# Kernel optimization log

Hardware: AMD Instinct MI355X
Metric: run time of the kernel (lower is better)

## Reference

```python
import jax, jax.numpy as jnp
import numpy as np

B, FEW, NSN, NQ, NN = 256, 5, 5, 10, 512
M, D, H, L, NSYM = 200, 100, 450, 2, 70000
BETA, MARGIN = 5.0, 1.0


def _lstm_dir(x, W_ih, W_hh, b_ih, b_hh):
    # x: (T, B, in) -> outputs (T, B, H), final h (B, H). PyTorch gate order i,f,g,o.
    Bn, Hn = x.shape[1], W_hh.shape[1]
    def cell(carry, xt):
        h, c = carry
        g = xt @ W_ih.T + h @ W_hh.T + b_ih + b_hh
        i, f, gg, o = jnp.split(g, 4, axis=-1)
        c = jax.nn.sigmoid(f) * c + jax.nn.sigmoid(i) * jnp.tanh(gg)
        h = jax.nn.sigmoid(o) * jnp.tanh(c)
        return (h, c), h
    z = jnp.zeros((Bn, Hn), x.dtype)
    (hT, _), ys = jax.lax.scan(cell, (z, z), x)
    return ys, hT


def _bidir(x, Wih, Whh, bih, bhh):
    # Wih: (2, 4H, in) stacked [fwd, bwd]
    yf, hf = _lstm_dir(x, Wih[0], Whh[0], bih[0], bhh[0])
    yb, hb = _lstm_dir(x[::-1], Wih[1], Whh[1], bih[1], bhh[1])
    return jnp.concatenate([yf, yb[::-1]], -1), hf, hb


def setup_inputs():
    key = jax.random.key(0)
    ks = jax.random.split(key, 30)
    f32 = jnp.float32
    emb = jax.random.normal(ks[0], (NSYM + 1, D), f32) * 0.1
    emb = emb.at[NSYM].set(0.0)  # padding_idx
    s = 0.05
    inp = dict(
        support=jax.random.normal(ks[1], (B, FEW, 2, D), f32),
        support_negative=jax.random.normal(ks[2], (B, NSN, 2, D), f32),
        query=jax.random.normal(ks[3], (B, NQ, 2, D), f32),
        negative=jax.random.normal(ks[4], (B, NN, 2, D), f32),
        norm_vector=jax.random.normal(ks[5], (B, 1, 1, D), f32),
        left_conn=jax.random.randint(ks[6], (FEW, B, M, 3), 0, NSYM, jnp.int32),
        right_conn=jax.random.randint(ks[7], (FEW, B, M, 3), 0, NSYM, jnp.int32),
        symbol_emb=emb,
        gcn_w=jax.random.normal(ks[8], (D, 2 * D), f32) * s,
        gcn_wb=jnp.zeros((D,), f32),
        gcn_b=jnp.zeros((D,), f32),
        attn_w=jax.random.normal(ks[9], (1, D), f32) * s,
        attn_wb=jnp.zeros((1,), f32),
        gate_w=jax.random.normal(ks[10], (1, D), f32) * s,
        gate_wb=jnp.zeros((1,), f32),
        gate_b=jnp.zeros((1,), f32),
        Wih0=jax.random.normal(ks[11], (2, 4 * H, 2 * D), f32) * s,
        Whh0=jax.random.normal(ks[12], (2, 4 * H, H), f32) * s,
        bih0=jnp.zeros((2, 4 * H), f32),
        bhh0=jnp.zeros((2, 4 * H), f32),
        Wih1=jax.random.normal(ks[13], (2, 4 * H, 2 * H), f32) * s,
        Whh1=jax.random.normal(ks[14], (2, 4 * H, H), f32) * s,
        bih1=jnp.zeros((2, 4 * H), f32),
        bhh1=jnp.zeros((2, 4 * H), f32),
        out_w=jax.random.normal(ks[15], (D, 2 * H * L), f32) * s,
        out_b=jnp.zeros((D,), f32),
    )
    return inp


def reference(support, support_negative, query, negative, norm_vector,
              left_conn, right_conn, symbol_emb,
              gcn_w, gcn_wb, gcn_b, attn_w, attn_wb, gate_w, gate_wb, gate_b,
              Wih0, Whh0, bih0, bhh0, Wih1, Whh1, bih1, bhh1, out_w, out_b):
    few, b, m, _ = left_conn.shape
    d = symbol_emb.shape[1]

    def neighbor_encoder(conn):  # (N, M, 3) -> (N, D); dropout=identity (eval)
        rel_e = symbol_emb[conn[:, :, 1]]            # (N, M, D)
        ent_e = symbol_emb[conn[:, :, 2]]            # (N, M, D)
        self_e = symbol_emb[conn[:, 0, 0]]           # (N, D)
        cat = jnp.concatenate([rel_e, ent_e], -1)    # (N, M, 2D)
        out = jax.nn.leaky_relu(cat @ gcn_w.T + gcn_wb + gcn_b, 0.01)
        attn = jax.nn.softmax(out @ attn_w.T + attn_wb, axis=1)  # (N, M, 1)
        out_attn = jnp.einsum('nmd,nm->nd', out, attn[..., 0])
        gate = jax.nn.sigmoid(out_attn @ gate_w.T + gate_wb + gate_b)  # (N, 1)
        return out_attn * gate + self_e * (1.0 - gate)

    # all (few, left/right) encodings in one fused pass
    conn_all = jnp.stack([left_conn, right_conn], 1).reshape(few * 2 * b, m, 3)
    enc = neighbor_encoder(conn_all).reshape(few, 2, b, d).transpose(2, 0, 1, 3)  # (B, few, 2, D)

    # LSTM_attn relation learner
    x = enc.reshape(b, few, 2 * d).transpose(1, 0, 2)  # (T=few, B, 2D)
    y, h0f, h0b = _bidir(x, Wih0, Whh0, bih0, bhh0)
    y, h1f, h1b = _bidir(y, Wih1, Whh1, bih1, bhh1)
    final = jnp.stack([h0f, h0b, h1f, h1b], 0)         # (2*L, B, H)
    output = y.transpose(1, 0, 2)                       # (B, T, 2H)
    hidden = final.reshape(-1, 2 * H, L)                # faithful to torch .view
    aw = jax.nn.softmax(jnp.einsum('bth,bhl->btl', output, hidden), axis=1)
    context = jnp.einsum('bth,btl->bhl', output, aw).reshape(b, 2 * H * L)
    rel = (context @ out_w.T + out_b).reshape(b, 1, 1, d)

    def split_concat(pos, neg):
        e1 = jnp.concatenate([pos[:, :, 0, :], neg[:, :, 0, :]], 1)[:, :, None, :]
        e2 = jnp.concatenate([pos[:, :, 1, :], neg[:, :, 1, :]], 1)[:, :, None, :]
        return e1, e2

    def emb_learner(h, t, r, norm, pos_num):
        norm = norm[:, :1, :, :]
        h = h - jnp.sum(h * norm, -1, keepdims=True) * norm
        t = t - jnp.sum(t * norm, -1, keepdims=True) * norm
        score = -jnp.linalg.norm(h + r - t, axis=-1)[:, :, 0]
        return score[:, :pos_num], score[:, pos_num:]

    nsn = support_negative.shape[1]
    def inner_loss(rel_):
        rel_s = jnp.broadcast_to(rel_, (b, few + nsn, 1, d))
        e1, e2 = split_concat(support, support_negative)
        p, n = emb_learner(e1, e2, rel_s, norm_vector, few)
        return jnp.mean(jax.nn.relu(MARGIN - (p - n)))

    grad_meta = jax.grad(inner_loss)(rel)
    rel_q = rel - BETA * grad_meta
    norm_q = norm_vector - BETA * grad_meta

    nq, nn = query.shape[1], negative.shape[1]
    e1, e2 = split_concat(query, negative)
    rel_qe = jnp.broadcast_to(rel_q, (b, nq + nn, 1, d))
    p_score, n_score = emb_learner(e1, e2, rel_qe, norm_q, nq)
    return p_score, n_score
```

## Files before the change

kernel.cpp:

```cpp
#include <hip/hip_runtime.h>

typedef unsigned short u16;
typedef unsigned int   u32;
typedef __attribute__((ext_vector_type(8))) short short8;
typedef __attribute__((ext_vector_type(4))) float f32x4;

__device__ __forceinline__ float u2f(u32 u){
  union { u32 i; float f; } v; v.i = u << 16; return v.f;
}
__device__ __forceinline__ u16 f2bu(float f){
  union { float f; u32 i; } v; v.f = f;
  u32 i = v.i;
  i += 0x7fffu + ((i >> 16) & 1u);
  return (u16)(i >> 16);
}
__device__ __forceinline__ float sigm(float x){ return 1.0f/(1.0f + expf(-x)); }
__device__ __forceinline__ float ldf(const void* p, size_t i, int bf){
  return bf ? u2f(((const u16*)p)[i]) : ((const float*)p)[i];
}
__device__ __forceinline__ float wsum(float v){
  #pragma unroll
  for (int off = 32; off > 0; off >>= 1) v += __shfl_xor(v, off, 64);
  return v;
}

__global__ __launch_bounds__(64) void k_detect(const u32* __restrict__ nv,
                                               int* __restrict__ flag)
{
  int i = threadIdx.x;
  u32 w = nv[i];
  u32 e = (w >> 7) & 0xffu;
  bool sane = (e >= 100u && e <= 140u);
  unsigned long long m = __ballot(sane);
  if (i == 0) *flag = (__popcll(m) >= 40) ? 1 : 0;
}

__global__ __launch_bounds__(256) void k_pack(
    const void* __restrict__ src, u16* __restrict__ dst,
    int K, int Kp, int R, int Rp, const int* __restrict__ flag)
{
  const int bf = *flag;
  int total = Rp*Kp;
  int idx = blockIdx.x*256 + threadIdx.x;
  if (idx >= total) return;
  int r = idx / Kp, k = idx - r*Kp;
  u16 v = 0;
  if (k < K && r < R){
    size_t si = (size_t)r*K + k;
    v = bf ? ((const u16*)src)[si] : f2bu(((const float*)src)[si]);
  }
  dst[idx] = v;
}

__global__ __launch_bounds__(256) void k_packe(
    const void* __restrict__ emb, u16* __restrict__ Eb,
    int total4, const int* __restrict__ flag)
{
  const int bf = *flag;
  int idx = blockIdx.x*256 + threadIdx.x;
  if (idx >= total4) return;
  size_t i = (size_t)idx*4;
  union { u16 q[4]; uint2 d; } o;
  if (bf){
    o.d = *(const uint2*)((const u16*)emb + i);
  } else {
    float4 t = *(const float4*)((const float*)emb + i);
    o.q[0] = f2bu(t.x); o.q[1] = f2bu(t.y);
    o.q[2] = f2bu(t.z); o.q[3] = f2bu(t.w);
  }
  *(uint2*)(Eb + i) = o.d;
}

__global__ __launch_bounds__(256) void k_packg(
    const void* __restrict__ src, u16* __restrict__ dst,
    int K, int Kp, const int* __restrict__ flag)
{
  const int bf = *flag;
  const int Kq = Kp >> 2;
  const int per = 1920*Kq;
  int idx = blockIdx.x*256 + threadIdx.x;
  if (idx >= 2*per) return;
  int z = idx / per, r = idx - z*per;
  int rp = r / Kq, cq = r - rp*Kq;
  int c0 = cq*4;
  int kblk = rp >> 6, rem = rp & 63, gate = rem >> 4, klo = rem & 15;
  int k = kblk*16 + klo;
  union { u16 q[4]; uint2 d; } o;
  o.q[0] = 0; o.q[1] = 0; o.q[2] = 0; o.q[3] = 0;
  if (k < 450){
    size_t base = ((size_t)z*1800 + (size_t)gate*450 + k)*K;
    #pragma unroll
    for (int e = 0; e < 4; ++e){
      int c = c0 + e;
      if (c < K)
        o.q[e] = bf ? ((const u16*)src)[base+c] : f2bu(((const float*)src)[base+c]);
    }
  }
  *(uint2*)(dst + (size_t)idx*4) = o.d;
}

__global__ __launch_bounds__(256) void k_packb(
    const void* __restrict__ bih, const void* __restrict__ bhh,
    float* __restrict__ Bp, const int* __restrict__ flag)
{
  const int bf = *flag;
  int idx = blockIdx.x*256 + threadIdx.x;
  if (idx >= 2*1920) return;
  int z = idx / 1920, rp = idx - z*1920;
  int kblk = rp >> 6, rem = rp & 63, gate = rem >> 4, klo = rem & 15;
  int k = kblk*16 + klo;
  float v = 0.0f;
  if (k < 450){
    size_t si = (size_t)z*1800 + (size_t)gate*450 + k;
    v = ldf(bih, si, bf) + ldf(bhh, si, bf);
  }
  Bp[idx] = v;
}

__global__ __launch_bounds__(512, 4) void k_gcn(
    const int* __restrict__ left, const int* __restrict__ right,
    const void* __restrict__ emb, const u16* __restrict__ Eb,
    const u16* __restrict__ Wg,
    const void* __restrict__ gcnwb, const void* __restrict__ gcnb,
    const void* __restrict__ attnw, const void* __restrict__ attnwb,
    const void* __restrict__ gatew, const void* __restrict__ gatewb,
    const void* __restrict__ gateb,
    const int* __restrict__ flag,
    u16* __restrict__ X0bf)
{
  __shared__ __align__(16) u16 As[208*40];
  __shared__ __align__(16) u16 Bs[112*232];
  __shared__ int c1_s[200], c2_s[200];
  __shared__ float logit_s[208];
  __shared__ float red_s[512];
  __shared__ float attnw_s[112], bias_s[112], gatew_s[112], oa_s[112];

  const int bf  = *flag;
  const int tid = threadIdx.x;
  const int n   = blockIdx.x;
  const int b   = n & 255;
  const int fs  = n >> 8;
  const int s   = fs & 1;
  const int f   = fs >> 1;
  const int* conn = (s == 0 ? left : right) + (size_t)(f*256 + b)*600;

  if (tid < 200){ c1_s[tid] = conn[tid*3+1]; c2_s[tid] = conn[tid*3+2]; }
  if (tid < 112){
    attnw_s[tid] = (tid < 100) ? ldf(attnw, tid, bf) : 0.0f;
    bias_s[tid]  = (tid < 100) ? (ldf(gcnwb, tid, bf) + ldf(gcnb, tid, bf)) : 0.0f;
    gatew_s[tid] = (tid < 100) ? ldf(gatew, tid, bf) : 0.0f;
    oa_s[tid] = 0.0f;
  }
  for (int g = tid; g < 112*28; g += 512){
    int r = g / 28, cc = g - r*28;
    *(short8*)(Bs + r*232 + cc*8) = *(const short8*)(Wg + (size_t)r*224 + cc*8);
  }
  __syncthreads();

  const int wid  = tid >> 6, lane = tid & 63, ln = lane & 15, quad = lane >> 4;
  const int mt0 = (wid < 5) ? 2*wid : (10 + (wid - 5));
  const int nmt = (wid < 5) ? 2 : 1;

  auto loadA = [&](int kc, uint2* pv){
    #pragma unroll
    for (int it = 0; it < 4; ++it){
      int g = tid + it*512;
      uint2 v; v.x = 0u; v.y = 0u;
      if (g < 1664){
        int r = g >> 3, gi = g & 7, k = kc*32 + gi*4;
        if (r < 200 && k < 200){
          int c  = (k < 100) ? c1_s[r] : c2_s[r];
          int kk = (k < 100) ? k : (k - 100);
          v = *(const uint2*)(Eb + (size_t)c*100 + kk);
        }
      }
      pv[it] = v;
    }
  };

  f32x4 acc[2][7];
  #pragma unroll
  for (int i = 0; i < 2; ++i)
    #pragma unroll
    for (int j = 0; j < 7; ++j) acc[i][j] = (f32x4)0.0f;

  uint2 pv[4];
  loadA(0, pv);

  for (int kc = 0; kc < 7; ++kc){
    const int k0 = kc*32;
    #pragma unroll
    for (int it = 0; it < 4; ++it){
      int g = tid + it*512;
      if (g < 1664){
        int r = g >> 3, gi = g & 7;
        *(uint2*)(As + r*40 + gi*4) = pv[it];
      }
    }
    __syncthreads();
    if (kc < 6) loadA(kc+1, pv);

    #pragma unroll
    for (int mi = 0; mi < 2; ++mi){
      if (mi < nmt){
        short8 afr = *(const short8*)(As + ((mt0+mi)*16 + ln)*40 + quad*8);
        #pragma unroll
        for (int nt = 0; nt < 7; ++nt){
          short8 bfr = *(const short8*)(Bs + (size_t)(nt*16 + ln)*232 + k0 + quad*8);
          acc[mi][nt] = __builtin_amdgcn_mfma_f32_16x16x32_bf16(afr, bfr, acc[mi][nt], 0, 0, 0);
        }
      }
    }
    __syncthreads();
  }

  const float awb = ldf(attnwb, 0, bf);
  #pragma unroll
  for (int mi = 0; mi < 2; ++mi){
    if (mi < nmt){
      #pragma unroll
      for (int rg = 0; rg < 4; ++rg){
        float p = 0.0f;
        #pragma unroll
        for (int nt = 0; nt < 7; ++nt){
          float x = acc[mi][nt][rg] + bias_s[nt*16 + ln];
          x = x > 0.0f ? x : 0.01f*x;
          p += x * attnw_s[nt*16 + ln];
        }
        p += __shfl_xor(p, 1, 64); p += __shfl_xor(p, 2, 64);
        p += __shfl_xor(p, 4, 64); p += __shfl_xor(p, 8, 64);
        int m = (mt0+mi)*16 + quad*4 + rg;
        if (ln == 0 && m < 200) logit_s[m] = p + awb;
      }
    }
  }
  __syncthreads();

  red_s[tid] = (tid < 200) ? logit_s[tid] : -3.0e38f;
  __syncthreads();
  for (int off = 256; off > 0; off >>= 1){
    if (tid < off) red_s[tid] = fmaxf(red_s[tid], red_s[tid+off]);
    __syncthreads();
  }
  float mx = red_s[0];
  __syncthreads();
  float ev = 0.0f;
  if (tid < 200) ev = expf(logit_s[tid] - mx);
  red_s[tid] = ev;
  __syncthreads();
  for (int off = 256; off > 0; off >>= 1){
    if (tid < off) red_s[tid] += red_s[tid+off];
    __syncthreads();
  }
  float S = red_s[0];
  __syncthreads();
  if (tid < 208) logit_s[tid] = (tid < 200) ? ev*(1.0f/S) : 0.0f;
  __syncthreads();

  float at[2][4];
  #pragma unroll
  for (int mi = 0; mi < 2; ++mi)
    #pragma unroll
    for (int rg = 0; rg < 4; ++rg)
      at[mi][rg] = (mi < nmt) ? logit_s[(mt0+mi)*16 + quad*4 + rg] : 0.0f;

  #pragma unroll
  for (int nt = 0; nt < 7; ++nt){
    float p = 0.0f;
    #pragma unroll
    for (int mi = 0; mi < 2; ++mi){
      if (mi < nmt){
        #pragma unroll
        for (int rg = 0; rg < 4; ++rg){
          float x = acc[mi][nt][rg] + bias_s[nt*16 + ln];
          x = x > 0.0f ? x : 0.01f*x;
          p += x * at[mi][rg];
        }
      }
    }
    p += __shfl_xor(p, 16, 64); p += __shfl_xor(p, 32, 64);
    if (quad == 0) atomicAdd(&oa_s[nt*16 + ln], p);
  }
  __syncthreads();

  red_s[tid] = (tid < 100) ? oa_s[tid]*gatew_s[tid] : 0.0f;
  __syncthreads();
  for (int off = 256; off > 0; off >>= 1){
    if (tid < off) red_s[tid] += red_s[tid+off];
    __syncthreads();
  }
  float gate = sigm(red_s[0] + ldf(gatewb, 0, bf) + ldf(gateb, 0, bf));
  if (tid < 100){
    int c0 = conn[0];
    float self = ldf(emb, (size_t)c0*100 + tid, bf);
    X0bf[((size_t)f*256 + b)*224 + s*100 + tid] = f2bu(oa_s[tid]*gate + self*(1.0f - gate));
  }
}

__global__ __launch_bounds__(256) void k_mgemm(
    const u16* __restrict__ A, int lda, size_t Astride,
    const u16* __restrict__ B, int ldb, size_t Bstride,
    const float* __restrict__ bsum,
    u16* __restrict__ out, size_t Ostride,
    int N, int KC)
{
  __shared__ __align__(16) u16 As[128*40];
  __shared__ __align__(16) u16 Bs[128*40];
  const int tid = threadIdx.x;
  const int z  = blockIdx.z;
  const int nb = blockIdx.x, mb = blockIdx.y;
  const u16* Az = A + (size_t)z*Astride;
  const u16* Bz = B + (size_t)z*Bstride;

  const int wid = tid >> 6, lane = tid & 63, ln = lane & 15, quad = lane >> 4;
  const int wm = wid >> 1, wn = wid & 1;

  f32x4 acc[4][4];
  #pragma unroll
  for (int i = 0; i < 4; ++i)
    #pragma unroll
    for (int j = 0; j < 4; ++j) acc[i][j] = (f32x4)0.0f;

  const int srow = tid >> 1;
  const int koff = (tid & 1)*16;
  const int rowA = mb*128 + srow;
  const int rowB = nb*128 + srow;

  for (int kc = 0; kc < KC; ++kc){
    const int k0 = kc*32 + koff;
    const u16* ap = Az + (size_t)rowA*lda + k0;
    const u16* bp = Bz + (size_t)rowB*ldb + k0;
    short8 av0 = *(const short8*)(ap);
    short8 av1 = *(const short8*)(ap + 8);
    short8 bv0 = *(const short8*)(bp);
    short8 bv1 = *(const short8*)(bp + 8);
    *(short8*)(As + srow*40 + koff)     = av0;
    *(short8*)(As + srow*40 + koff + 8) = av1;
    *(short8*)(Bs + srow*40 + koff)     = bv0;
    *(short8*)(Bs + srow*40 + koff + 8) = bv1;
    __syncthreads();
    short8 af[4], bfr[4];
    #pragma unroll
    for (int i = 0; i < 4; ++i)
      af[i] = *(const short8*)(As + (wm*64 + i*16 + ln)*40 + quad*8);
    #pragma unroll
    for (int j = 0; j < 4; ++j)
      bfr[j] = *(const short8*)(Bs + (wn*64 + j*16 + ln)*40 + quad*8);
    #pragma unroll
    for (int i = 0; i < 4; ++i)
      #pragma unroll
      for (int j = 0; j < 4; ++j)
        acc[i][j] = __builtin_amdgcn_mfma_f32_16x16x32_bf16(af[i], bfr[j], acc[i][j], 0, 0, 0);
    __syncthreads();
  }

  #pragma unroll
  for (int j = 0; j < 4; ++j){
    int col = nb*128 + wn*64 + j*16 + ln;
    float bias = bsum ? bsum[(size_t)z*1920 + col] : 0.0f;
    #pragma unroll
    for (int i = 0; i < 4; ++i){
      #pragma unroll
      for (int rg = 0; rg < 4; ++rg){
        int row = mb*128 + wm*64 + i*16 + quad*4 + rg;
        out[(size_t)z*Ostride + (size_t)row*N + col] = f2bu(acc[i][j][rg] + bias);
      }
    }
  }
}

__global__ __launch_bounds__(256) void k_hstep(
    const u16* __restrict__ Hin, const u16* __restrict__ Whp,
    const u16* __restrict__ Gb, float* __restrict__ HC,
    u16* __restrict__ Hout, u16* __restrict__ Ybf, float* __restrict__ Yf,
    float* __restrict__ HF, int s, int layer)
{
  __shared__ __align__(16) u16 As[32*40];
  __shared__ __align__(16) u16 Bs[128*40];
  const int tid = threadIdx.x;
  const int nb = blockIdx.x, mb = blockIdx.y, z = blockIdx.z;
  const int wid = tid >> 6, lane = tid & 63, ln = lane & 15, quad = lane >> 4;
  const int wm = wid >> 1, wn = wid & 1;

  const u16* Az = Hin + ((size_t)z*256 + mb*32)*480;
  const u16* Bz = Whp + (size_t)z*1920*480 + (size_t)nb*128*480;

  f32x4 acc[4];
  #pragma unroll
  for (int j = 0; j < 4; ++j) acc[j] = (f32x4)0.0f;

  const int ar = tid >> 2, ap = tid & 3;
  const int br = tid >> 1, bp = tid & 1;
  for (int kc = 0; kc < 15; ++kc){
    const int k0 = kc*32;
    if (tid < 128)
      *(short8*)(As + ar*40 + ap*8) = *(const short8*)(Az + (size_t)ar*480 + k0 + ap*8);
    *(short8*)(Bs + br*40 + bp*16)     = *(const short8*)(Bz + (size_t)br*480 + k0 + bp*16);
    *(short8*)(Bs + br*40 + bp*16 + 8) = *(const short8*)(Bz + (size_t)br*480 + k0 + bp*16 + 8);
    __syncthreads();
    short8 afr = *(const short8*)(As + (wm*16 + ln)*40 + quad*8);
    #pragma unroll
    for (int j = 0; j < 4; ++j){
      short8 bfr = *(const short8*)(Bs + (wn*64 + j*16 + ln)*40 + quad*8);
      acc[j] = __builtin_amdgcn_mfma_f32_16x16x32_bf16(afr, bfr, acc[j], 0, 0, 0);
    }
    __syncthreads();
  }

  const int kblk = nb*2 + wn;
  const int k = kblk*16 + ln;
  const int t = z ? (4 - s) : s;
  if (k < 450){
    const u16* Gz = Gb + (size_t)z*2457600 + (size_t)t*256*1920;
    #pragma unroll
    for (int rg = 0; rg < 4; ++rg){
      int b = mb*32 + wm*16 + quad*4 + rg;
      const u16* grow = Gz + (size_t)b*1920 + nb*128 + wn*64 + ln;
      float gi = acc[0][rg] + u2f(grow[0]);
      float gf = acc[1][rg] + u2f(grow[16]);
      float gg = acc[2][rg] + u2f(grow[32]);
      float go = acc[3][rg] + u2f(grow[48]);
      float* cp = HC + ((size_t)(2+z)*256 + b)*450 + k;
      float c = sigm(gf)*(*cp) + sigm(gi)*tanhf(gg);
      float h = sigm(go)*tanhf(c);
      *cp = c;
      Hout[((size_t)z*256 + b)*480 + k] = f2bu(h);
      if (Ybf) Ybf[((size_t)t*256 + b)*928 + z*450 + k] = f2bu(h);
      else     Yf [((size_t)t*256 + b)*900 + z*450 + k] = h;
      HF[((size_t)(layer*2+z)*256 + b)*450 + k] = h;
    }
  }
}

__global__ __launch_bounds__(256) void k_attn(
    const float* __restrict__ Y1, const float* __restrict__ HF,
    float* __restrict__ CTX)
{
  __shared__ float red2[40];
  __shared__ float aw[10];
  int b = blockIdx.x, tid = threadIdx.x;
  int wid = tid >> 6, lane = tid & 63;
  for (int p = 0; p < 10; ++p){
    int t = p >> 1, l = p & 1;
    float a = 0.0f;
    for (int h = tid; h < 900; h += 256)
      a += Y1[((size_t)t*256 + b)*900 + h] * HF[(size_t)b*1800 + h*2 + l];
    a = wsum(a);
    if (lane == 0) red2[p*4 + wid] = a;
  }
  __syncthreads();
  if (tid < 2){
    int l = tid;
    float sc[5];
    float mxv = -3.0e38f;
    for (int t = 0; t < 5; ++t){
      int p = t*2 + l;
      sc[t] = red2[p*4] + red2[p*4+1] + red2[p*4+2] + red2[p*4+3];
      mxv = fmaxf(mxv, sc[t]);
    }
    float e[5], sum = 0.0f;
    for (int t = 0; t < 5; ++t){ e[t] = expf(sc[t]-mxv); sum += e[t]; }
    for (int t = 0; t < 5; ++t) aw[t*2+l] = e[t]/sum;
  }
  __syncthreads();
  for (int h = tid; h < 900; h += 256){
    float v0 = 0.0f, v1 = 0.0f;
    for (int t = 0; t < 5; ++t){
      float y = Y1[((size_t)t*256 + b)*900 + h];
      v0 += y*aw[t*2+0]; v1 += y*aw[t*2+1];
    }
    CTX[(size_t)b*1800 + h*2 + 0] = v0;
    CTX[(size_t)b*1800 + h*2 + 1] = v1;
  }
}

__global__ __launch_bounds__(256) void k_gemm(
    const float* __restrict__ A, const void* __restrict__ W, size_t wEl,
    const void* __restrict__ b1, const void* __restrict__ b2, size_t bEl,
    const int* __restrict__ flag,
    float* __restrict__ out, int K, int C)
{
  extern __shared__ float a_s[];
  const int bf = *flag;
  const int tid = threadIdx.x;
  const int r = blockIdx.y;
  const float* a = A + (size_t)r*K;
  for (int k = tid; k < K; k += 256) a_s[k] = a[k];
  __syncthreads();
  const int j = blockIdx.x*256 + tid;
  if (j >= C) return;
  float acc = 0.0f;
  if (b1) acc += ldf(b1, bEl + j, bf);
  if (b2) acc += ldf(b2, bEl + j, bf);
  if (bf){
    const u16* w = (const u16*)W + wEl + (size_t)j*K;
    for (int k = 0; k < K; k += 4){
      uint2 wv = *(const uint2*)(w + k);
      acc += a_s[k]   * u2f(wv.x & 0xffffu);
      acc += a_s[k+1] * u2f(wv.x >> 16);
      acc += a_s[k+2] * u2f(wv.y & 0xffffu);
      acc += a_s[k+3] * u2f(wv.y >> 16);
    }
  } else {
    const float* w = (const float*)W + wEl + (size_t)j*K;
    for (int k = 0; k < K; k += 4){
      float4 wv = *(const float4*)(w + k);
      acc += a_s[k]*wv.x + a_s[k+1]*wv.y + a_s[k+2]*wv.z + a_s[k+3]*wv.w;
    }
  }
  out[(size_t)r*C + j] = acc;
}

__global__ __launch_bounds__(64) void k_grad(
    const void* __restrict__ sup, const void* __restrict__ supn,
    const void* __restrict__ normv, const float* __restrict__ REL,
    const int* __restrict__ flag,
    float* __restrict__ RELQ, float* __restrict__ NORMQ)
{
  const int bf = *flag;
  const int b = blockIdx.x, lane = threadIdx.x;
  const int d0 = lane, d1 = lane + 64;
  const bool a1 = (d1 < 100);
  float nv0 = ldf(normv, (size_t)b*100 + d0, bf);
  float nv1 = a1 ? ldf(normv, (size_t)b*100 + d1, bf) : 0.0f;
  float rl0 = REL[(size_t)b*100 + d0];
  float rl1 = a1 ? REL[(size_t)b*100 + d1] : 0.0f;
  float acc0 = 0.0f, acc1 = 0.0f;
  for (int j = 0; j < 5; ++j){
    size_t base = (size_t)(b*5+j)*200;
    float h10 = ldf(sup,  base + d0, bf);
    float t10 = ldf(sup,  base + 100 + d0, bf);
    float h20 = ldf(supn, base + d0, bf);
    float t20 = ldf(supn, base + 100 + d0, bf);
    float h11 = a1 ? ldf(sup,  base + d1, bf) : 0.0f;
    float t11 = a1 ? ldf(sup,  base + 100 + d1, bf) : 0.0f;
    float h21 = a1 ? ldf(supn, base + d1, bf) : 0.0f;
    float t21 = a1 ? ldf(supn, base + 100 + d1, bf) : 0.0f;
    float hd1 = wsum(h10*nv0 + h11*nv1);
    float td1 = wsum(t10*nv0 + t11*nv1);
    float hd2 = wsum(h20*nv0 + h21*nv1);
    float td2 = wsum(t20*nv0 + t21*nv1);
    float upd0 = (h10 - hd1*nv0) + rl0 - (t10 - td1*nv0);
    float upd1 = (h11 - hd1*nv1) + rl1 - (t11 - td1*nv1);
    float und0 = (h20 - hd2*nv0) + rl0 - (t20 - td2*nv0);
    float und1 = (h21 - hd2*nv1) + rl1 - (t21 - td2*nv1);
    if (!a1){ upd1 = 0.0f; und1 = 0.0f; }
    float np2 = wsum(upd0*upd0 + upd1*upd1);
    float nn2 = wsum(und0*und0 + und1*und1);
    float p = -sqrtf(np2), nsc = -sqrtf(nn2);
    if (1.0f - (p - nsc) > 0.0f){
      float ip = 1.0f/sqrtf(np2), in = 1.0f/sqrtf(nn2);
      acc0 += upd0*ip - und0*in;
      acc1 += upd1*ip - und1*in;
    }
  }
  float g0 = acc0 * (1.0f/1280.0f);
  RELQ [(size_t)b*100 + d0] = rl0 - 5.0f*g0;
  NORMQ[(size_t)b*100 + d0] = nv0 - 5.0f*g0;
  if (a1){
    float g1 = acc1 * (1.0f/1280.0f);
    RELQ [(size_t)b*100 + d1] = rl1 - 5.0f*g1;
    NORMQ[(size_t)b*100 + d1] = nv1 - 5.0f*g1;
  }
}

__global__ __launch_bounds__(256) void k_score(
    const void* __restrict__ query, const void* __restrict__ neg,
    const float* __restrict__ RELQ, const float* __restrict__ NORMQ,
    const int* __restrict__ flag, void* __restrict__ out)
{
  __shared__ __align__(16) float nq[104], rq[104];
  const int bf = *flag;
  const int b = blockIdx.x, tid = threadIdx.x;
  if (tid < 100){ nq[tid] = NORMQ[b*100+tid]; rq[tid] = RELQ[b*100+tid]; }
  __syncthreads();
  const int wid = tid >> 6, lane = tid & 63;
  const bool lo = (lane < 25);
  const bool hi = (lane >= 32 && lane < 57);
  const int d0 = lo ? lane*4 : (hi ? (lane-32)*4 : 0);
  float4 w4 = make_float4(0.0f,0.0f,0.0f,0.0f);
  float4 r4 = make_float4(0.0f,0.0f,0.0f,0.0f);
  if (lo || hi) w4 = *(const float4*)(nq + d0);
  if (lo)       r4 = *(const float4*)(rq + d0);

  for (int qi = blockIdx.y*4 + wid; qi < 522; qi += 32){
    const void* src = (qi < 10) ? query : neg;
    size_t row = (qi < 10) ? ((size_t)b*10 + qi) : ((size_t)b*512 + qi - 10);
    size_t base = row*200 + (hi ? 100 : 0) + d0;
    float4 v = make_float4(0.0f,0.0f,0.0f,0.0f);
    if (lo || hi){
      if (bf){
        uint2 u = *(const uint2*)((const u16*)src + base);
        v.x = u2f(u.x & 0xffffu); v.y = u2f(u.x >> 16);
        v.z = u2f(u.y & 0xffffu); v.w = u2f(u.y >> 16);
      } else {
        v = *(const float4*)((const float*)src + base);
      }
    }
    float pr = v.x*w4.x + v.y*w4.y + v.z*w4.z + v.w*w4.w;
    #pragma unroll
    for (int off = 16; off > 0; off >>= 1) pr += __shfl_xor(pr, off, 32);
    float tdv = __shfl(pr, lane + 32, 64);
    float4 t4;
    t4.x = __shfl(v.x, lane + 32, 64);
    t4.y = __shfl(v.y, lane + 32, 64);
    t4.z = __shfl(v.z, lane + 32, 64);
    t4.w = __shfl(v.w, lane + 32, 64);
    float s2 = 0.0f;
    if (lo){
      float ux = (v.x - pr*w4.x) + r4.x - (t4.x - tdv*w4.x);
      float uy = (v.y - pr*w4.y) + r4.y - (t4.y - tdv*w4.y);
      float uz = (v.z - pr*w4.z) + r4.z - (t4.z - tdv*w4.z);
      float uw = (v.w - pr*w4.w) + r4.w - (t4.w - tdv*w4.w);
      s2 = ux*ux + uy*uy + uz*uz + uw*uw;
    }
    #pragma unroll
    for (int off = 16; off > 0; off >>= 1) s2 += __shfl_xor(s2, off, 32);
    if (lane == 0){
      float sc = -sqrtf(s2);
      size_t oi = (qi < 10) ? ((size_t)b*10 + qi) : (2560 + (size_t)b*512 + (qi - 10));
      if (bf) ((u16*)out)[oi] = f2bu(sc);
      else    ((float*)out)[oi] = sc;
    }
  }
}

extern "C" void kernel_launch(void* const* d_in, const int* in_sizes, int n_in,
                              void* d_out, int out_size, void* d_ws, size_t ws_size,
                              hipStream_t stream)
{
  const void* support = d_in[0];
  const void* supneg  = d_in[1];
  const void* query   = d_in[2];
  const void* negat   = d_in[3];
  const void* normv   = d_in[4];
  const int* left     = (const int*)d_in[5];
  const int* right    = (const int*)d_in[6];
  const void* emb     = d_in[7];
  const void* gcnw    = d_in[8];
  const void* gcnwb   = d_in[9];
  const void* gcnb    = d_in[10];
  const void* attnw   = d_in[11];
  const void* attnwb  = d_in[12];
  const void* gatew   = d_in[13];
  const void* gatewb  = d_in[14];
  const void* gateb   = d_in[15];
  const void* Wih0    = d_in[16];
  const void* Whh0    = d_in[17];
  const void* bih0    = d_in[18];
  const void* bhh0    = d_in[19];
  const void* Wih1    = d_in[20];
  const void* Whh1    = d_in[21];
  const void* bih1    = d_in[22];
  const void* bhh1    = d_in[23];
  const void* outw    = d_in[24];
  const void* outb    = d_in[25];

  int*   dflag = (int*)d_ws;
  float* fws   = (float*)d_ws + 16;
  float* Y1   = fws;
  float* HF   = Y1 + 1152000;
  float* HC   = HF + 460800;
  float* CTX  = HC + 460800;
  float* RELb = CTX + 460800;
  float* RELQ = RELb + 25600;
  float* NORMQ= RELQ + 25600;
  float* Bp   = NORMQ + 25600;
  float* fend = Bp + 3840;
  u16* Gb   = (u16*)fend;
  u16* X0bf = Gb + 4915200;
  u16* Y0bf = X0bf + 286720;
  u16* Hbf  = Y0bf + 1187840;
  u16* Wg   = Hbf + 491520;
  u16* Eb   = Wg + 25088;
  u16* Wp   = Eb;
  u16* Whp  = Eb + 3563520;

  k_detect<<<1, 64, 0, stream>>>((const u32*)normv, dflag);

  hipMemsetAsync(X0bf, 0, 286720*sizeof(u16), stream);
  k_pack<<<(112*224+255)/256, 256, 0, stream>>>(gcnw, Wg, 200, 224, 100, 112, dflag);
  k_packe<<<(1750025+255)/256, 256, 0, stream>>>(emb, Eb, 1750025, dflag);
  k_gcn<<<2560, 512, 0, stream>>>(left, right, emb, Eb, Wg, gcnwb, gcnb,
                                  attnw, attnwb, gatew, gatewb, gateb,
                                  dflag, X0bf);

  u16* Hpar0 = Hbf;
  u16* Hpar1 = Hbf + 245760;

  hipMemsetAsync(Y0bf, 0, 1187840*sizeof(u16), stream);
  hipMemsetAsync(Hbf, 0, 491520*sizeof(u16), stream);
  hipMemsetAsync(HC, 0, 460800*sizeof(float), stream);
  k_packg<<<(2*1920*224/4+255)/256, 256, 0, stream>>>(Wih0, Wp, 200, 224, dflag);
  k_packg<<<(2*1920*480/4+255)/256, 256, 0, stream>>>(Whh0, Whp, 450, 480, dflag);
  k_packb<<<15, 256, 0, stream>>>(bih0, bhh0, Bp, dflag);
  k_mgemm<<<dim3(15,10,2), 256, 0, stream>>>(
      X0bf, 224, 0, Wp, 224, (size_t)1920*224,
      Bp, Gb, 2457600, 1920, 7);
  {
    u16* hc = Hpar0; u16* hn = Hpar1;
    for (int s = 0; s < 5; ++s){
      k_hstep<<<dim3(15,8,2), 256, 0, stream>>>(hc, Whp, Gb, HC, hn,
                                                Y0bf, nullptr, HF, s, 0);
      u16* tmp = hc; hc = hn; hn = tmp;
    }
  }

  hipMemsetAsync(Hbf, 0, 491520*sizeof(u16), stream);
  hipMemsetAsync(HC, 0, 460800*sizeof(float), stream);
  k_packg<<<(2*1920*928/4+255)/256, 256, 0, stream>>>(Wih1, Wp, 900, 928, dflag);
  k_packg<<<(2*1920*480/4+255)/256, 256, 0, stream>>>(Whh1, Whp, 450, 480, dflag);
  k_packb<<<15, 256, 0, stream>>>(bih1, bhh1, Bp, dflag);
  k_mgemm<<<dim3(15,10,2), 256, 0, stream>>>(
      Y0bf, 928, 0, Wp, 928, (size_t)1920*928,
      Bp, Gb, 2457600, 1920, 29);
  {
    u16* hc = Hpar0; u16* hn = Hpar1;
    for (int s = 0; s < 5; ++s){
      k_hstep<<<dim3(15,8,2), 256, 0, stream>>>(hc, Whp, Gb, HC, hn,
                                                nullptr, Y1, HF, s, 1);
      u16* tmp = hc; hc = hn; hn = tmp;
    }
  }

  k_attn<<<256, 256, 0, stream>>>(Y1, HF, CTX);
  k_gemm<<<dim3(1,256), 256, 1800*4, stream>>>(CTX, outw, 0, outb, nullptr, 0,
                                               dflag, RELb, 1800, 100);
  k_grad<<<256, 64, 0, stream>>>(support, supneg, normv, RELb, dflag, RELQ, NORMQ);
  k_score<<<dim3(256,8), 256, 0, stream>>>(query, negat, RELQ, NORMQ, dflag, d_out);
}
```

Measured before the change: 726.1 us.

## Fuse LSTM recurrent steps into persistent kernel with grid barrier

```diff
diff --git a/kernel.cpp b/kernel.cpp
--- a/kernel.cpp
+++ b/kernel.cpp
@@ -369,66 +369,85 @@
   }
 }
 
-__global__ __launch_bounds__(256) void k_hstep(
-    const u16* __restrict__ Hin, const u16* __restrict__ Whp,
-    const u16* __restrict__ Gb, float* __restrict__ HC,
-    u16* __restrict__ Hout, u16* __restrict__ Ybf, float* __restrict__ Yf,
-    float* __restrict__ HF, int s, int layer)
-{
-  __shared__ __align__(16) u16 As[32*40];
-  __shared__ __align__(16) u16 Bs[128*40];
+__global__ __launch_bounds__(256) void k_hchain(
+    const u16* __restrict__ Whp, const u16* __restrict__ Gb,
+    float* __restrict__ HC, u16* __restrict__ H0, u16* __restrict__ H1,
+    u16* __restrict__ Ybf, float* __restrict__ Yf, float* __restrict__ HF,
+    int layer, int* __restrict__ bar)
+{
+  extern __shared__ __align__(16) u16 smem[];
+  u16* Bsp = smem;
+  u16* Asp = smem + 128*488;
   const int tid = threadIdx.x;
   const int nb = blockIdx.x, mb = blockIdx.y, z = blockIdx.z;
   const int wid = tid >> 6, lane = tid & 63, ln = lane & 15, quad = lane >> 4;
   const int wm = wid >> 1, wn = wid & 1;
 
-  const u16* Az = Hin + ((size_t)z*256 + mb*32)*480;
   const u16* Bz = Whp + (size_t)z*1920*480 + (size_t)nb*128*480;
-
-  f32x4 acc[4];
-  #pragma unroll
-  for (int j = 0; j < 4; ++j) acc[j] = (f32x4)0.0f;
-
-  const int ar = tid >> 2, ap = tid & 3;
-  const int br = tid >> 1, bp = tid & 1;
-  for (int kc = 0; kc < 15; ++kc){
-    const int k0 = kc*32;
-    if (tid < 128)
-      *(short8*)(As + ar*40 + ap*8) = *(const short8*)(Az + (size_t)ar*480 + k0 + ap*8);
-    *(short8*)(Bs + br*40 + bp*16)     = *(const short8*)(Bz + (size_t)br*480 + k0 + bp*16);
-    *(short8*)(Bs + br*40 + bp*16 + 8) = *(const short8*)(Bz + (size_t)br*480 + k0 + bp*16 + 8);
-    __syncthreads();
-    short8 afr = *(const short8*)(As + (wm*16 + ln)*40 + quad*8);
-    #pragma unroll
-    for (int j = 0; j < 4; ++j){
-      short8 bfr = *(const short8*)(Bs + (wn*64 + j*16 + ln)*40 + quad*8);
-      acc[j] = __builtin_amdgcn_mfma_f32_16x16x32_bf16(afr, bfr, acc[j], 0, 0, 0);
-    }
-    __syncthreads();
+  for (int g = tid; g < 128*60; g += 256){
+    int r = g/60, cc = g - r*60;
+    *(short8*)(Bsp + r*488 + cc*8) = *(const short8*)(Bz + (size_t)r*480 + cc*8);
   }
 
   const int kblk = nb*2 + wn;
   const int k = kblk*16 + ln;
-  const int t = z ? (4 - s) : s;
-  if (k < 450){
-    const u16* Gz = Gb + (size_t)z*2457600 + (size_t)t*256*1920;
-    #pragma unroll
-    for (int rg = 0; rg < 4; ++rg){
-      int b = mb*32 + wm*16 + quad*4 + rg;
-      const u16* grow = Gz + (size_t)b*1920 + nb*128 + wn*64 + ln;
-      float gi = acc[0][rg] + u2f(grow[0]);
-      float gf = acc[1][rg] + u2f(grow[16]);
-      float gg = acc[2][rg] + u2f(grow[32]);
-      float go = acc[3][rg] + u2f(grow[48]);
-      float* cp = HC + ((size_t)(2+z)*256 + b)*450 + k;
-      float c = sigm(gf)*(*cp) + sigm(gi)*tanhf(gg);
-      float h = sigm(go)*tanhf(c);
-      *cp = c;
-      Hout[((size_t)z*256 + b)*480 + k] = f2bu(h);
-      if (Ybf) Ybf[((size_t)t*256 + b)*928 + z*450 + k] = f2bu(h);
-      else     Yf [((size_t)t*256 + b)*900 + z*450 + k] = h;
-      HF[((size_t)(layer*2+z)*256 + b)*450 + k] = h;
-    }
+
+  const u16* Hin = H0;
+  u16* Hout = H1;
+  for (int s = 0; s < 5; ++s){
+    const u16* Az = Hin + ((size_t)z*256 + mb*32)*480;
+    for (int g = tid; g < 32*60; g += 256){
+      int r = g/60, cc = g - r*60;
+      *(short8*)(Asp + r*488 + cc*8) = *(const short8*)(Az + (size_t)r*480 + cc*8);
+    }
+    __syncthreads();
+
+    f32x4 acc[4];
+    #pragma unroll
+    for (int j = 0; j < 4; ++j) acc[j] = (f32x4)0.0f;
+    for (int kc = 0; kc < 15; ++kc){
+      short8 afr = *(const short8*)(Asp + (size_t)(wm*16 + ln)*488 + kc*32 + quad*8);
+      #pragma unroll
+      for (int j = 0; j < 4; ++j){
+        short8 bfr = *(const short8*)(Bsp + (size_t)(wn*64 + j*16 + ln)*488 + kc*32 + quad*8);
+        acc[j] = __builtin_amdgcn_mfma_f32_16x16x32_bf16(afr, bfr, acc[j], 0, 0, 0);
+      }
+    }
+
+    const int t = z ? (4 - s) : s;
+    if (k < 450){
+      const u16* Gz = Gb + (size_t)z*2457600 + (size_t)t*256*1920;
+      #pragma unroll
+      for (int rg = 0; rg < 4; ++rg){
+        int b = mb*32 + wm*16 + quad*4 + rg;
+        const u16* grow = Gz + (size_t)b*1920 + nb*128 + wn*64 + ln;
+        float gi = acc[0][rg] + u2f(grow[0]);
+        float gf = acc[1][rg] + u2f(grow[16]);
+        float gg = acc[2][rg] + u2f(grow[32]);
+        float go = acc[3][rg] + u2f(grow[48]);
+        float* cp = HC + ((size_t)(2+z)*256 + b)*450 + k;
+        float c = sigm(gf)*(*cp) + sigm(gi)*tanhf(gg);
+        float h = sigm(go)*tanhf(c);
+        *cp = c;
+        Hout[((size_t)z*256 + b)*480 + k] = f2bu(h);
+        if (Ybf) Ybf[((size_t)t*256 + b)*928 + z*450 + k] = f2bu(h);
+        else     Yf [((size_t)t*256 + b)*900 + z*450 + k] = h;
+        HF[((size_t)(layer*2+z)*256 + b)*450 + k] = h;
+      }
+    }
+
+    if (s < 4){
+      __syncthreads();
+      if (tid == 0){
+        __threadfence();
+        atomicAdd(bar, 1);
+        int target = 240*(s+1);
+        while (atomicAdd(bar, 0) < target) __builtin_amdgcn_s_sleep(16);
+        __threadfence();
+      }
+      __syncthreads();
+    }
+    const u16* tmp = Hin; Hin = Hout; Hout = (u16*)tmp;
   }
 }
 
@@ -657,6 +676,7 @@
   const void* outb    = d_in[25];
 
   int*   dflag = (int*)d_ws;
+  int*   dbar  = dflag + 2;
   float* fws   = (float*)d_ws + 16;
   float* Y1   = fws;
   float* HF   = Y1 + 1152000;
@@ -676,6 +696,7 @@
   u16* Wp   = Eb;
   u16* Whp  = Eb + 3563520;
 
+  hipMemsetAsync(dbar, 0, 2*sizeof(int), stream);
   k_detect<<<1, 64, 0, stream>>>((const u32*)normv, dflag);
 
   hipMemsetAsync(X0bf, 0, 286720*sizeof(u16), stream);
@@ -687,6 +708,7 @@
 
   u16* Hpar0 = Hbf;
   u16* Hpar1 = Hbf + 245760;
+  const size_t HCHAIN_LDS = (size_t)(128+32)*488*sizeof(u16);
 
   hipMemsetAsync(Y0bf, 0, 1187840*sizeof(u16), stream);
   hipMemsetAsync(Hbf, 0, 491520*sizeof(u16), stream);
@@ -697,14 +719,8 @@
   k_mgemm<<<dim3(15,10,2), 256, 0, stream>>>(
       X0bf, 224, 0, Wp, 224, (size_t)1920*224,
       Bp, Gb, 2457600, 1920, 7);
-  {
-    u16* hc = Hpar0; u16* hn = Hpar1;
-    for (int s = 0; s < 5; ++s){
-      k_hstep<<<dim3(15,8,2), 256, 0, stream>>>(hc, Whp, Gb, HC, hn,
-                                                Y0bf, nullptr, HF, s, 0);
-      u16* tmp = hc; hc = hn; hn = tmp;
-    }
-  }
+  k_hchain<<<dim3(15,8,2), 256, HCHAIN_LDS, stream>>>(
+      Whp, Gb, HC, Hpar0, Hpar1, Y0bf, nullptr, HF, 0, dbar);
 
   hipMemsetAsync(Hbf, 0, 491520*sizeof(u16), stream);
   hipMemsetAsync(HC, 0, 460800*sizeof(float), stream);
@@ -714,14 +730,8 @@
   k_mgemm<<<dim3(15,10,2), 256, 0, stream>>>(
       Y0bf, 928, 0, Wp, 928, (size_t)1920*928,
       Bp, Gb, 2457600, 1920, 29);
-  {
-    u16* hc = Hpar0; u16* hn = Hpar1;
-    for (int s = 0; s < 5; ++s){
-      k_hstep<<<dim3(15,8,2), 256, 0, stream>>>(hc, Whp, Gb, HC, hn,
-                                                nullptr, Y1, HF, s, 1);
-      u16* tmp = hc; hc = hn; hn = tmp;
-    }
-  }
+  k_hchain<<<dim3(15,8,2), 256, HCHAIN_LDS, stream>>>(
+      Whp, Gb, HC, Hpar0, Hpar1, nullptr, Y1, HF, 1, dbar + 1);
 
   k_attn<<<256, 256, 0, stream>>>(Y1, HF, CTX);
   k_gemm<<<dim3(1,256), 256, 1800*4, stream>>>(CTX, outw, 0, outb, nullptr, 0,
```

Measured after the change: 809.7 us. 1.12x slower.

## Restructure LSTM step kernel into single-wave blocks loading MFMA fragments directly

Applied to the files above, without the earlier changes.

```diff
diff --git a/kernel.cpp b/kernel.cpp
--- a/kernel.cpp
+++ b/kernel.cpp
@@ -369,53 +369,44 @@
   }
 }
 
-__global__ __launch_bounds__(256) void k_hstep(
+__global__ __launch_bounds__(64) void k_hstep(
     const u16* __restrict__ Hin, const u16* __restrict__ Whp,
     const u16* __restrict__ Gb, float* __restrict__ HC,
     u16* __restrict__ Hout, u16* __restrict__ Ybf, float* __restrict__ Yf,
     float* __restrict__ HF, int s, int layer)
 {
-  __shared__ __align__(16) u16 As[32*40];
-  __shared__ __align__(16) u16 Bs[128*40];
-  const int tid = threadIdx.x;
-  const int nb = blockIdx.x, mb = blockIdx.y, z = blockIdx.z;
-  const int wid = tid >> 6, lane = tid & 63, ln = lane & 15, quad = lane >> 4;
-  const int wm = wid >> 1, wn = wid & 1;
-
-  const u16* Az = Hin + ((size_t)z*256 + mb*32)*480;
-  const u16* Bz = Whp + (size_t)z*1920*480 + (size_t)nb*128*480;
+  const int lane = threadIdx.x;
+  const int ln = lane & 15, quad = lane >> 4;
+  const int kb = blockIdx.x;
+  const int mb = blockIdx.y;
+  const int z  = blockIdx.z;
+
+  const u16* Az = Hin + ((size_t)z*256 + mb*16)*480;
+  const u16* Bz = Whp + (size_t)z*1920*480 + (size_t)kb*64*480;
 
   f32x4 acc[4];
   #pragma unroll
   for (int j = 0; j < 4; ++j) acc[j] = (f32x4)0.0f;
 
-  const int ar = tid >> 2, ap = tid & 3;
-  const int br = tid >> 1, bp = tid & 1;
+  #pragma unroll
   for (int kc = 0; kc < 15; ++kc){
-    const int k0 = kc*32;
-    if (tid < 128)
-      *(short8*)(As + ar*40 + ap*8) = *(const short8*)(Az + (size_t)ar*480 + k0 + ap*8);
-    *(short8*)(Bs + br*40 + bp*16)     = *(const short8*)(Bz + (size_t)br*480 + k0 + bp*16);
-    *(short8*)(Bs + br*40 + bp*16 + 8) = *(const short8*)(Bz + (size_t)br*480 + k0 + bp*16 + 8);
-    __syncthreads();
-    short8 afr = *(const short8*)(As + (wm*16 + ln)*40 + quad*8);
+    const int k0 = kc*32 + quad*8;
+    short8 afr = *(const short8*)(Az + (size_t)ln*480 + k0);
     #pragma unroll
     for (int j = 0; j < 4; ++j){
-      short8 bfr = *(const short8*)(Bs + (wn*64 + j*16 + ln)*40 + quad*8);
+      short8 bfr = *(const short8*)(Bz + (size_t)(j*16 + ln)*480 + k0);
       acc[j] = __builtin_amdgcn_mfma_f32_16x16x32_bf16(afr, bfr, acc[j], 0, 0, 0);
     }
-    __syncthreads();
-  }
-
-  const int kblk = nb*2 + wn;
-  const int k = kblk*16 + ln;
+  }
+
+  const int k = kb*16 + ln;
   const int t = z ? (4 - s) : s;
   if (k < 450){
     const u16* Gz = Gb + (size_t)z*2457600 + (size_t)t*256*1920;
     #pragma unroll
     for (int rg = 0; rg < 4; ++rg){
-      int b = mb*32 + wm*16 + quad*4 + rg;
-      const u16* grow = Gz + (size_t)b*1920 + nb*128 + wn*64 + ln;
+      int b = mb*16 + quad*4 + rg;
+      const u16* grow = Gz + (size_t)b*1920 + kb*64 + ln;
       float gi = acc[0][rg] + u2f(grow[0]);
       float gf = acc[1][rg] + u2f(grow[16]);
       float gg = acc[2][rg] + u2f(grow[32]);
@@ -700,7 +691,7 @@
   {
     u16* hc = Hpar0; u16* hn = Hpar1;
     for (int s = 0; s < 5; ++s){
-      k_hstep<<<dim3(15,8,2), 256, 0, stream>>>(hc, Whp, Gb, HC, hn,
+      k_hstep<<<dim3(30,16,2), 64, 0, stream>>>(hc, Whp, Gb, HC, hn,
                                                 Y0bf, nullptr, HF, s, 0);
       u16* tmp = hc; hc = hn; hn = tmp;
     }
@@ -717,7 +708,7 @@
   {
     u16* hc = Hpar0; u16* hn = Hpar1;
     for (int s = 0; s < 5; ++s){
-      k_hstep<<<dim3(15,8,2), 256, 0, stream>>>(hc, Whp, Gb, HC, hn,
+      k_hstep<<<dim3(30,16,2), 64, 0, stream>>>(hc, Whp, Gb, HC, hn,
                                                 nullptr, Y1, HF, s, 1);
       u16* tmp = hc; hc = hn; hn = tmp;
     }
```

Result: faster. 684.6 us (-5.7%).
